# Kernel tuning notes

Hardware: AMD Instinct MI355X
Metric: run time of the kernel (lower is better)

The kernel has to match this reference:

```python
import jax, jax.numpy as jnp
import numpy as np

EMBED_DIM = 128
NUM_HEADS = 8
HEAD_DIM = EMBED_DIM // NUM_HEADS
SCALE = float(np.sqrt(HEAD_DIM))


def setup_inputs() -> dict:
    key = jax.random.key(0)
    ks = jax.random.split(key, 16)
    B, N, M, E = 16, 256, 256, EMBED_DIM
    s = 1.0 / np.sqrt(E)
    inp = {
        "query": jax.random.normal(ks[0], (B, N, E), jnp.float32),
        "key": jax.random.normal(ks[1], (B, M, E), jnp.float32),
        "value": jax.random.normal(ks[2], (B, M, E), jnp.float32),
        "rel_pe": jax.random.normal(ks[3], (B, N, M, E), jnp.float32),
        "attn_mask": jnp.zeros((B, N, M), jnp.float32),
        # linear params stored as [in, out]; y = x @ W + b
        "Wq": jax.random.normal(ks[4], (E, E), jnp.float32) * s,
        "bq": jnp.zeros((E,), jnp.float32),
        "Wk": jax.random.normal(ks[5], (E, E), jnp.float32) * s,
        "bk": jnp.zeros((E,), jnp.float32),
        "Wv": jax.random.normal(ks[6], (E, E), jnp.float32) * s,
        "bv": jnp.zeros((E,), jnp.float32),
        "Wpe": jax.random.normal(ks[7], (E, E), jnp.float32) * s,
        "bpe": jnp.zeros((E,), jnp.float32),
        "Wo": jax.random.normal(ks[8], (E, E), jnp.float32) * s,
        "bo": jnp.zeros((E,), jnp.float32),
    }
    return inp


def reference(query, key, value, rel_pe, attn_mask,
              Wq, bq, Wk, bk, Wv, bv, Wpe, bpe, Wo, bo):
    B, N, E = query.shape
    M = key.shape[1]
    H, D = NUM_HEADS, HEAD_DIM
    q = (query @ Wq + bq).reshape(B, N, H, D)
    k = (key @ Wk + bk).reshape(B, M, H, D)
    v = (value @ Wv + bv).reshape(B, M, H, D)
    pe = (rel_pe @ Wpe + bpe).reshape(B, N, M, H, D)
    score = jnp.einsum('bnhd,bmhd->bhnm', q, k) \
          + jnp.einsum('bnhd,bnmhd->bhnm', q, pe)
    score = score / SCALE + attn_mask[:, None, :, :]
    attn = jax.nn.softmax(score, axis=-1)
    attn = jnp.nan_to_num(attn, nan=0.0)  # dropout is identity in eval mode
    out = jnp.einsum('bhnm,bmhd->bnhd', attn, v) \
        + jnp.einsum('bhnm,bnmhd->bnhd', attn, pe)
    out = out.reshape(B, N, E)
    return out @ Wo + bo
```

## Files before the change

kernel.cpp:

```cpp
#include <hip/hip_runtime.h>
#include <hip/hip_bf16.h>
#include <math.h>

typedef __attribute__((ext_vector_type(8))) short bf16x8;
typedef __attribute__((ext_vector_type(4))) float f32x4;

__device__ __forceinline__ void wg_barrier() {
    asm volatile("s_waitcnt lgkmcnt(0)" ::: "memory");
    __builtin_amdgcn_s_barrier();
    asm volatile("" ::: "memory");
}

__global__ void qkv_proj_kernel(const float* __restrict__ query,
                                const float* __restrict__ key,
                                const float* __restrict__ value,
                                const float* __restrict__ Wq, const float* __restrict__ bq,
                                const float* __restrict__ Wk, const float* __restrict__ bk,
                                const float* __restrict__ Wv, const float* __restrict__ bv,
                                float* __restrict__ qf, float* __restrict__ kf,
                                float* __restrict__ vf)
{
    const int mat = blockIdx.x >> 8;
    const int rb  = blockIdx.x & 255;
    const float* X; const float* W; const float* bias; float* dst;
    if (mat == 0)      { X = query; W = Wq; bias = bq; dst = qf; }
    else if (mat == 1) { X = key;   W = Wk; bias = bk; dst = kf; }
    else               { X = value; W = Wv; bias = bv; dst = vf; }

    __shared__ float sX[16][128];
    const int tid = threadIdx.x;
    const float* src = X + (size_t)rb * 16 * 128;
    #pragma unroll
    for (int i = 0; i < 8; ++i) {
        int idx = tid + i * 256;
        sX[idx >> 7][idx & 127] = src[idx];
    }
    __syncthreads();

    const int col = tid & 127;
    const int rg  = tid >> 7;
    float acc[8] = {0.f,0.f,0.f,0.f,0.f,0.f,0.f,0.f};
    for (int e = 0; e < 128; ++e) {
        float w = W[e * 128 + col];
        #pragma unroll
        for (int r = 0; r < 8; ++r) acc[r] += sX[rg * 8 + r][e] * w;
    }
    float bb = bias[col];
    #pragma unroll
    for (int r = 0; r < 8; ++r)
        dst[(size_t)(rb * 16 + rg * 8 + r) * 128 + col] = acc[r] + bb;
}

__global__ __launch_bounds__(256) void mha_main_kernel(
    const float* __restrict__ relpe,
    const float* __restrict__ mask,
    const float* __restrict__ qf,
    const float* __restrict__ kf,
    const float* __restrict__ vf,
    const float* __restrict__ Wpe, const float* __restrict__ bpe,
    const float* __restrict__ Wo,  const float* __restrict__ bo,
    float* __restrict__ out)
{
    __shared__ __hip_bfloat16 sA[64][140];
    __shared__ __hip_bfloat16 sWt[16][136];
    __shared__ __hip_bfloat16 sPfull[16][264];
    __shared__ float sQK[256][9];
    __shared__ float sQs[128];
    __shared__ float sLw[32];
    __shared__ float sL[8];
    __shared__ float sRed[128];
    __shared__ float sOutF[128];
    __shared__ float sPrE[8][132];

    const int tid  = threadIdx.x;
    const int lane = tid & 63;
    const int wv   = tid >> 6;
    const int bid  = ((blockIdx.x & 7) << 9) | (blockIdx.x >> 3);
    const int b    = bid >> 8;
    const int n    = bid & 255;
    const size_t bn = (size_t)(b * 256 + n);

    float4 pf[8];
    {
        const float4* s4 = (const float4*)(relpe + (bn * 256) * 128);
        #pragma unroll
        for (int i = 0; i < 8; ++i) pf[i] = s4[tid + i * 256];
    }

    if (tid < 128) sQs[tid] = qf[bn * 128 + tid] * 0.25f;
    #pragma unroll
    for (int j = 0; j < 8; ++j) sPfull[8 + j][tid] = __float2bfloat16(0.f);
    if (tid < 128) {
        #pragma unroll
        for (int r = 8; r < 16; ++r) sWt[r][tid] = __float2bfloat16(0.f);
    }
    wg_barrier();

    #pragma unroll
    for (int o = tid; o < 1024; o += 256) {
        int h = o >> 7, e = o & 127;
        const float4* wr = (const float4*)(Wpe + (size_t)e * 128 + h * 16);
        float4 w0 = wr[0], w1 = wr[1], w2 = wr[2], w3 = wr[3];
        const float* qh = &sQs[h * 16];
        float acc = w0.x*qh[0]+w0.y*qh[1]+w0.z*qh[2]+w0.w*qh[3]
                  + w1.x*qh[4]+w1.y*qh[5]+w1.z*qh[6]+w1.w*qh[7]
                  + w2.x*qh[8]+w2.y*qh[9]+w2.z*qh[10]+w2.w*qh[11]
                  + w3.x*qh[12]+w3.y*qh[13]+w3.z*qh[14]+w3.w*qh[15];
        sWt[h][e] = __float2bfloat16(acc);
    }

    {
        const int hsc = tid >> 5, ml = tid & 31;
        float cb = 0.f;
        #pragma unroll
        for (int d = 0; d < 16; ++d) cb += bpe[hsc * 16 + d] * sQs[hsc * 16 + d];
        #pragma unroll
        for (int i = 0; i < 8; ++i) {
            int m = i * 32 + ml;
            const float4* k4 = (const float4*)(kf + ((size_t)(b * 256) + m) * 128 + hsc * 16);
            float4 ka = k4[0], kb = k4[1], kc = k4[2], kd = k4[3];
            const float* qh = &sQs[hsc * 16];
            float s = ka.x*qh[0]+ka.y*qh[1]+ka.z*qh[2]+ka.w*qh[3]
                    + kb.x*qh[4]+kb.y*qh[5]+kb.z*qh[6]+kb.w*qh[7]
                    + kc.x*qh[8]+kc.y*qh[9]+kc.z*qh[10]+kc.w*qh[11]
                    + kd.x*qh[12]+kd.y*qh[13]+kd.z*qh[14]+kd.w*qh[15];
            sQK[m][hsc] = s + cb + mask[bn * 256 + m];
        }
    }

    #pragma unroll
    for (int i = 0; i < 8; ++i) {
        int idx4 = tid + i * 256;
        int lr = idx4 >> 5, c4 = (idx4 & 31) * 4;
        union { __hip_bfloat162 h2[2]; uint2 u; } pk;
        pk.h2[0] = __float22bfloat162_rn(make_float2(pf[i].x, pf[i].y));
        pk.h2[1] = __float22bfloat162_rn(make_float2(pf[i].z, pf[i].w));
        *(uint2*)&sA[lr][c4] = pk.u;
    }
    wg_barrier();

    float l_acc = 0.f;
    f32x4 pr0 = {}, pr1 = {};
    const int arow = lane & 15;
    const int koff = lane >> 4;

    #pragma unroll 1
    for (int t = 0; t < 4; ++t) {
        if (t < 3) {
            const float4* s4 = (const float4*)(relpe + (bn * 256 + (t + 1) * 64) * 128);
            #pragma unroll
            for (int i = 0; i < 8; ++i) pf[i] = s4[tid + i * 256];
        }

        f32x4 cs;
        #pragma unroll
        for (int r = 0; r < 4; ++r) {
            int m = t * 64 + wv * 16 + koff * 4 + r;
            cs[r] = (arow < 8) ? sQK[m][arow] : 0.f;
        }
        #pragma unroll
        for (int kt = 0; kt < 4; ++kt) {
            bf16x8 af  = *(const bf16x8*)&sA[wv * 16 + arow][kt * 32 + koff * 8];
            bf16x8 bfr = *(const bf16x8*)&sWt[arow][kt * 32 + koff * 8];
            cs = __builtin_amdgcn_mfma_f32_16x16x32_bf16(af, bfr, cs, 0, 0, 0);
        }

        if (arow < 8) {
            float p0 = __expf(cs[0]), p1 = __expf(cs[1]);
            float p2 = __expf(cs[2]), p3 = __expf(cs[3]);
            l_acc += (p0 + p1) + (p2 + p3);
            union { __hip_bfloat162 h2[2]; uint2 u; } pk;
            pk.h2[0] = __float22bfloat162_rn(make_float2(p0, p1));
            pk.h2[1] = __float22bfloat162_rn(make_float2(p2, p3));
            *(uint2*)&sPfull[arow][t * 64 + wv * 16 + koff * 4] = pk.u;
        }
        wg_barrier();

        #pragma unroll
        for (int kt = 0; kt < 2; ++kt) {
            bf16x8 ap = *(const bf16x8*)&sPfull[arow][t * 64 + kt * 32 + koff * 8];
            bf16x8 b0, b1;
            #pragma unroll
            for (int j = 0; j < 8; ++j) {
                int row = kt * 32 + koff * 8 + j;
                b0[j] = *(const short*)&sA[row][wv * 32 + arow];
                b1[j] = *(const short*)&sA[row][wv * 32 + 16 + arow];
            }
            pr0 = __builtin_amdgcn_mfma_f32_16x16x32_bf16(ap, b0, pr0, 0, 0, 0);
            pr1 = __builtin_amdgcn_mfma_f32_16x16x32_bf16(ap, b1, pr1, 0, 0, 0);
        }
        wg_barrier();

        if (t < 3) {
            #pragma unroll
            for (int i = 0; i < 8; ++i) {
                int idx4 = tid + i * 256;
                int lr = idx4 >> 5, c4 = (idx4 & 31) * 4;
                union { __hip_bfloat162 h2[2]; uint2 u; } pk;
                pk.h2[0] = __float22bfloat162_rn(make_float2(pf[i].x, pf[i].y));
                pk.h2[1] = __float22bfloat162_rn(make_float2(pf[i].z, pf[i].w));
                *(uint2*)&sA[lr][c4] = pk.u;
            }
            wg_barrier();
        }
    }

    {
        float lw = l_acc;
        lw += __shfl_xor(lw, 16);
        lw += __shfl_xor(lw, 32);
        if (koff == 0 && arow < 8) sLw[wv * 8 + arow] = lw;
    }
    #pragma unroll
    for (int r = 0; r < 4; ++r) {
        int hh = koff * 4 + r;
        if (hh < 8) {
            sPrE[hh][wv * 32 + arow]      = pr0[r];
            sPrE[hh][wv * 32 + 16 + arow] = pr1[r];
        }
    }
    __syncthreads();
    if (tid < 8) sL[tid] = sLw[tid] + sLw[8 + tid] + sLw[16 + tid] + sLw[24 + tid];
    __syncthreads();

    const int e = tid & 127, half = tid >> 7, hh2 = e >> 4;

    float oa = 0.f;
    {
        const float* vp = vf + ((size_t)(b * 256) + half * 128) * 128 + e;
        const __hip_bfloat16* pp = &sPfull[hh2][half * 128];
        #pragma unroll 8
        for (int mm = 0; mm < 128; ++mm)
            oa += __bfloat162float(pp[mm]) * vp[(size_t)mm * 128];
    }
    float ype = 0.f;
    {
        const float* wp  = Wpe + (size_t)(half * 64) * 128 + e;
        const float* prh = &sPrE[hh2][half * 64];
        #pragma unroll 8
        for (int ee = 0; ee < 64; ++ee) ype += prh[ee] * wp[(size_t)ee * 128];
    }
    if (half) sRed[e] = oa + ype;
    __syncthreads();
    if (!half) sOutF[e] = (oa + ype + sRed[e]) / sL[hh2] + bpe[e];
    __syncthreads();

    float y = 0.f;
    {
        const float* wo = Wo + (size_t)(half * 64) * 128 + e;
        #pragma unroll 8
        for (int ee = 0; ee < 64; ++ee) y += sOutF[half * 64 + ee] * wo[(size_t)ee * 128];
    }
    if (half) sRed[e] = y;
    __syncthreads();
    if (!half) out[bn * 128 + e] = y + sRed[e] + bo[e];
}

extern "C" void kernel_launch(void* const* d_in, const int* in_sizes, int n_in,
                              void* d_out, int out_size, void* d_ws, size_t ws_size,
                              hipStream_t stream)
{
    const float* query = (const float*)d_in[0];
    const float* key   = (const float*)d_in[1];
    const float* value = (const float*)d_in[2];
    const float* relpe = (const float*)d_in[3];
    const float* mask  = (const float*)d_in[4];
    const float* Wq  = (const float*)d_in[5];
    const float* bq  = (const float*)d_in[6];
    const float* Wk  = (const float*)d_in[7];
    const float* bk  = (const float*)d_in[8];
    const float* Wv  = (const float*)d_in[9];
    const float* bv  = (const float*)d_in[10];
    const float* Wpe = (const float*)d_in[11];
    const float* bpe = (const float*)d_in[12];
    const float* Wo  = (const float*)d_in[13];
    const float* bo  = (const float*)d_in[14];
    float* out = (float*)d_out;

    float* qf = (float*)d_ws;
    float* kf = qf + 16 * 256 * 128;
    float* vf = kf + 16 * 256 * 128;

    qkv_proj_kernel<<<dim3(768), dim3(256), 0, stream>>>(
        query, key, value, Wq, bq, Wk, bk, Wv, bv, qf, kf, vf);
    mha_main_kernel<<<dim3(4096), dim3(256), 0, stream>>>(
        relpe, mask, qf, kf, vf, Wpe, bpe, Wo, bo, out);
}
```

Before: 224.6 us.

## Stream rel_pe tiles into double-buffered LDS with async global_load_lds

Replaces the register-staged rel_pe prefetch, which converted each tile to bf16 and wrote it into shared memory, with direct global-to-LDS loads of the raw fp32 tiles. The tiles go into two XOR-swizzled buffers, and the bf16 conversion moves to fragment-read time just before each MFMA. A partial vmcnt wait lets the next tile's load overlap the current tile's score and PE-accumulation MFMAs. Score and other scratch arrays are aliased into the buffers, and zero-fill of unused padding rows is dropped. The cost is about 79KB of dynamic shared memory per block, which lowers occupancy, plus repeated fp32-to-bf16 conversion during the strided reads.

```diff
diff --git a/kernel.cpp b/kernel.cpp
--- a/kernel.cpp
+++ b/kernel.cpp
@@ -9,6 +9,22 @@
     asm volatile("s_waitcnt lgkmcnt(0)" ::: "memory");
     __builtin_amdgcn_s_barrier();
     asm volatile("" ::: "memory");
+}
+
+__device__ __forceinline__ bf16x8 pack_f32x8(float4 a, float4 b) {
+    union { __hip_bfloat162 h2[4]; bf16x8 v; } u;
+    u.h2[0] = __float22bfloat162_rn(make_float2(a.x, a.y));
+    u.h2[1] = __float22bfloat162_rn(make_float2(a.z, a.w));
+    u.h2[2] = __float22bfloat162_rn(make_float2(b.x, b.y));
+    u.h2[3] = __float22bfloat162_rn(make_float2(b.z, b.w));
+    return u.v;
+}
+__device__ __forceinline__ bf16x8 pack_f32p(const float* f) {
+    union { __hip_bfloat162 h2[4]; bf16x8 v; } u;
+    #pragma unroll
+    for (int k = 0; k < 4; ++k)
+        u.h2[k] = __float22bfloat162_rn(make_float2(f[2*k], f[2*k+1]));
+    return u.v;
 }
 
 __global__ void qkv_proj_kernel(const float* __restrict__ query,
@@ -40,6 +56,7 @@
     const int col = tid & 127;
     const int rg  = tid >> 7;
     float acc[8] = {0.f,0.f,0.f,0.f,0.f,0.f,0.f,0.f};
+    #pragma unroll 8
     for (int e = 0; e < 128; ++e) {
         float w = W[e * 128 + col];
         #pragma unroll
@@ -50,6 +67,69 @@
     for (int r = 0; r < 8; ++r)
         dst[(size_t)(rb * 16 + rg * 8 + r) * 128 + col] = acc[r] + bb;
 }
+
+
+#define STAGE(dstbuf, gbase)                                                      \
+    {                                                                             \
+        _Pragma("unroll")                                                         \
+        for (int i_ = 0; i_ < 8; ++i_) {                                          \
+            int row_ = (i_ * 4 + wv) * 2 + (lane >> 5);                           \
+            int goff_ = row_ * 512 + (((lane & 31) ^ (row_ & 7)) << 4);           \
+            __builtin_amdgcn_global_load_lds(                                     \
+                (const __attribute__((address_space(1))) void*)((gbase) + goff_), \
+                (__attribute__((address_space(3))) void*)((dstbuf) + (i_ * 4 + wv) * 1024), \
+                16, 0, 0);                                                        \
+        }                                                                         \
+        __builtin_amdgcn_sched_barrier(0);                                        \
+    }
+
+#define TILE_STEP(T, CURB, NXTB, WAITSTR)                                         \
+    {                                                                             \
+        if ((T) < 3) STAGE(NXTB, relpe_b + ((T) + 1) * 32768)                     \
+        asm volatile("s_waitcnt " WAITSTR ::: "memory");                          \
+        __builtin_amdgcn_sched_barrier(0);                                        \
+        wg_barrier();                                                             \
+        const char* bA_ = (CURB);                                                 \
+                                              \
+        f32x4 cs;                                                                 \
+        cs[0] = qkr[(T)*4+0]; cs[1] = qkr[(T)*4+1];                               \
+        cs[2] = qkr[(T)*4+2]; cs[3] = qkr[(T)*4+3];                               \
+        _Pragma("unroll")                                                         \
+        for (int kt = 0; kt < 4; ++kt) {                                          \
+            int u0 = kt * 8 + koff * 2;                                           \
+            float4 fa0 = *(const float4*)(bA_ + rowa_b + ((u0 ^ xr) << 4));       \
+            float4 fa1 = *(const float4*)(bA_ + rowa_b + (((u0 + 1) ^ xr) << 4)); \
+            bf16x8 af = pack_f32x8(fa0, fa1);                                     \
+            bf16x8 bw = *(const bf16x8*)&sWt[arow][kt * 32 + koff * 8];           \
+            cs = __builtin_amdgcn_mfma_f32_16x16x32_bf16(af, bw, cs, 0, 0, 0);    \
+        }                                                                         \
+        if (arow < 8) {                                                           \
+            float p0 = __expf(cs[0]), p1 = __expf(cs[1]);                         \
+            float p2 = __expf(cs[2]), p3 = __expf(cs[3]);                         \
+            l_acc += (p0 + p1) + (p2 + p3);                                       \
+            union { __hip_bfloat162 h2[2]; uint2 u; } pk;                         \
+            pk.h2[0] = __float22bfloat162_rn(make_float2(p0, p1));                \
+            pk.h2[1] = __float22bfloat162_rn(make_float2(p2, p3));                \
+            *(uint2*)&sPfull[arow][(T) * 64 + wv * 16 + koff * 4] = pk.u;         \
+        }                                                                         \
+        wg_barrier();                                                             \
+                                               \
+        _Pragma("unroll")                                                         \
+        for (int kt = 0; kt < 2; ++kt) {                                          \
+            bf16x8 ap = *(const bf16x8*)&sPfull[arow][(T) * 64 + kt * 32 + koff * 8]; \
+            float f0[8], f1[8];                                                   \
+            _Pragma("unroll")                                                     \
+            for (int j = 0; j < 8; ++j) {                                         \
+                int rb_ = kt * 16384 + koff * 4096 + j * 512;                     \
+                f0[j] = *(const float*)(bA_ + rb_ + ((colu0 ^ j) << 4) + colw0);  \
+                f1[j] = *(const float*)(bA_ + rb_ + ((colu1 ^ j) << 4) + colw0);  \
+            }                                                                     \
+            bf16x8 b0 = pack_f32p(f0), b1 = pack_f32p(f1);                        \
+            pr0 = __builtin_amdgcn_mfma_f32_16x16x32_bf16(ap, b0, pr0, 0, 0, 0);  \
+            pr1 = __builtin_amdgcn_mfma_f32_16x16x32_bf16(ap, b1, pr1, 0, 0, 0);  \
+        }                                                                         \
+        wg_barrier();                                                             \
+    }
 
 __global__ __launch_bounds__(256) void mha_main_kernel(
     const float* __restrict__ relpe,
@@ -61,16 +141,14 @@
     const float* __restrict__ Wo,  const float* __restrict__ bo,
     float* __restrict__ out)
 {
-    __shared__ __hip_bfloat16 sA[64][140];
-    __shared__ __hip_bfloat16 sWt[16][136];
-    __shared__ __hip_bfloat16 sPfull[16][264];
-    __shared__ float sQK[256][9];
-    __shared__ float sQs[128];
-    __shared__ float sLw[32];
-    __shared__ float sL[8];
-    __shared__ float sRed[128];
-    __shared__ float sOutF[128];
-    __shared__ float sPrE[8][132];
+    extern __shared__ char smem[];
+    char* buf0 = smem;
+    char* buf1 = smem + 32768;
+    __hip_bfloat16 (*sPfull)[264] = (__hip_bfloat16(*)[264])(smem + 65536);
+    __hip_bfloat16 (*sWt)[136]    = (__hip_bfloat16(*)[136])(smem + 73984);
+    float* sQs = (float*)(smem + 78336);
+    float* sLw = (float*)(smem + 78848);
+    float* sL  = (float*)(smem + 78976);
 
     const int tid  = threadIdx.x;
     const int lane = tid & 63;
@@ -79,21 +157,14 @@
     const int b    = bid >> 8;
     const int n    = bid & 255;
     const size_t bn = (size_t)(b * 256 + n);
-
-    float4 pf[8];
-    {
-        const float4* s4 = (const float4*)(relpe + (bn * 256) * 128);
-        #pragma unroll
-        for (int i = 0; i < 8; ++i) pf[i] = s4[tid + i * 256];
-    }
+    const int arow = lane & 15;
+    const int koff = lane >> 4;
+
+    const char* relpe_b = (const char*)relpe + bn * 131072;
+
+    STAGE(buf0, relpe_b)
 
     if (tid < 128) sQs[tid] = qf[bn * 128 + tid] * 0.25f;
-    #pragma unroll
-    for (int j = 0; j < 8; ++j) sPfull[8 + j][tid] = __float2bfloat16(0.f);
-    if (tid < 128) {
-        #pragma unroll
-        for (int r = 8; r < 16; ++r) sWt[r][tid] = __float2bfloat16(0.f);
-    }
     wg_barrier();
 
     #pragma unroll
@@ -109,6 +180,7 @@
         sWt[h][e] = __float2bfloat16(acc);
     }
 
+    float (*sQK)[9] = (float(*)[9])buf1;
     {
         const int hsc = tid >> 5, ml = tid & 31;
         float cb = 0.f;
@@ -127,83 +199,29 @@
             sQK[m][hsc] = s + cb + mask[bn * 256 + m];
         }
     }
-
-    #pragma unroll
-    for (int i = 0; i < 8; ++i) {
-        int idx4 = tid + i * 256;
-        int lr = idx4 >> 5, c4 = (idx4 & 31) * 4;
-        union { __hip_bfloat162 h2[2]; uint2 u; } pk;
-        pk.h2[0] = __float22bfloat162_rn(make_float2(pf[i].x, pf[i].y));
-        pk.h2[1] = __float22bfloat162_rn(make_float2(pf[i].z, pf[i].w));
-        *(uint2*)&sA[lr][c4] = pk.u;
-    }
+    wg_barrier();
+
+    float qkr[16];
+    #pragma unroll
+    for (int t2 = 0; t2 < 4; ++t2)
+        #pragma unroll
+        for (int r = 0; r < 4; ++r)
+            qkr[t2 * 4 + r] = (arow < 8)
+                ? sQK[t2 * 64 + wv * 16 + koff * 4 + r][arow] : 0.f;
     wg_barrier();
 
     float l_acc = 0.f;
     f32x4 pr0 = {}, pr1 = {};
-    const int arow = lane & 15;
-    const int koff = lane >> 4;
-
-    #pragma unroll 1
-    for (int t = 0; t < 4; ++t) {
-        if (t < 3) {
-            const float4* s4 = (const float4*)(relpe + (bn * 256 + (t + 1) * 64) * 128);
-            #pragma unroll
-            for (int i = 0; i < 8; ++i) pf[i] = s4[tid + i * 256];
-        }
-
-        f32x4 cs;
-        #pragma unroll
-        for (int r = 0; r < 4; ++r) {
-            int m = t * 64 + wv * 16 + koff * 4 + r;
-            cs[r] = (arow < 8) ? sQK[m][arow] : 0.f;
-        }
-        #pragma unroll
-        for (int kt = 0; kt < 4; ++kt) {
-            bf16x8 af  = *(const bf16x8*)&sA[wv * 16 + arow][kt * 32 + koff * 8];
-            bf16x8 bfr = *(const bf16x8*)&sWt[arow][kt * 32 + koff * 8];
-            cs = __builtin_amdgcn_mfma_f32_16x16x32_bf16(af, bfr, cs, 0, 0, 0);
-        }
-
-        if (arow < 8) {
-            float p0 = __expf(cs[0]), p1 = __expf(cs[1]);
-            float p2 = __expf(cs[2]), p3 = __expf(cs[3]);
-            l_acc += (p0 + p1) + (p2 + p3);
-            union { __hip_bfloat162 h2[2]; uint2 u; } pk;
-            pk.h2[0] = __float22bfloat162_rn(make_float2(p0, p1));
-            pk.h2[1] = __float22bfloat162_rn(make_float2(p2, p3));
-            *(uint2*)&sPfull[arow][t * 64 + wv * 16 + koff * 4] = pk.u;
-        }
-        wg_barrier();
-
-        #pragma unroll
-        for (int kt = 0; kt < 2; ++kt) {
-            bf16x8 ap = *(const bf16x8*)&sPfull[arow][t * 64 + kt * 32 + koff * 8];
-            bf16x8 b0, b1;
-            #pragma unroll
-            for (int j = 0; j < 8; ++j) {
-                int row = kt * 32 + koff * 8 + j;
-                b0[j] = *(const short*)&sA[row][wv * 32 + arow];
-                b1[j] = *(const short*)&sA[row][wv * 32 + 16 + arow];
-            }
-            pr0 = __builtin_amdgcn_mfma_f32_16x16x32_bf16(ap, b0, pr0, 0, 0, 0);
-            pr1 = __builtin_amdgcn_mfma_f32_16x16x32_bf16(ap, b1, pr1, 0, 0, 0);
-        }
-        wg_barrier();
-
-        if (t < 3) {
-            #pragma unroll
-            for (int i = 0; i < 8; ++i) {
-                int idx4 = tid + i * 256;
-                int lr = idx4 >> 5, c4 = (idx4 & 31) * 4;
-                union { __hip_bfloat162 h2[2]; uint2 u; } pk;
-                pk.h2[0] = __float22bfloat162_rn(make_float2(pf[i].x, pf[i].y));
-                pk.h2[1] = __float22bfloat162_rn(make_float2(pf[i].z, pf[i].w));
-                *(uint2*)&sA[lr][c4] = pk.u;
-            }
-            wg_barrier();
-        }
-    }
+    const int rowa_b = (wv * 16 + arow) * 512;
+    const int xr     = (wv * 16 + arow) & 7;
+    const int colu0  = (wv * 32 + arow) >> 2;
+    const int colw0  = ((wv * 32 + arow) & 3) * 4;
+    const int colu1  = colu0 + 4;
+
+    TILE_STEP(0, buf0, buf1, "vmcnt(8)")
+    TILE_STEP(1, buf1, buf0, "vmcnt(8)")
+    TILE_STEP(2, buf0, buf1, "vmcnt(8)")
+    TILE_STEP(3, buf1, buf0, "vmcnt(0)")
 
     {
         float lw = l_acc;
@@ -211,12 +229,15 @@
         lw += __shfl_xor(lw, 32);
         if (koff == 0 && arow < 8) sLw[wv * 8 + arow] = lw;
     }
+    float* sPrE = (float*)buf0;
+    float* sRed = (float*)(buf0 + 4352);
+    float* sOutF= (float*)(buf0 + 4864);
     #pragma unroll
     for (int r = 0; r < 4; ++r) {
         int hh = koff * 4 + r;
         if (hh < 8) {
-            sPrE[hh][wv * 32 + arow]      = pr0[r];
-            sPrE[hh][wv * 32 + 16 + arow] = pr1[r];
+            sPrE[hh * 132 + wv * 32 + arow]      = pr0[r];
+            sPrE[hh * 132 + wv * 32 + 16 + arow] = pr1[r];
         }
     }
     __syncthreads();
@@ -236,7 +257,7 @@
     float ype = 0.f;
     {
         const float* wp  = Wpe + (size_t)(half * 64) * 128 + e;
-        const float* prh = &sPrE[hh2][half * 64];
+        const float* prh = &sPrE[hh2 * 132 + half * 64];
         #pragma unroll 8
         for (int ee = 0; ee < 64; ++ee) ype += prh[ee] * wp[(size_t)ee * 128];
     }
@@ -281,8 +302,12 @@
     float* kf = qf + 16 * 256 * 128;
     float* vf = kf + 16 * 256 * 128;
 
+    static bool attr_done = false;
+    (void)hipFuncSetAttribute((const void*)mha_main_kernel,
+                              hipFuncAttributeMaxDynamicSharedMemorySize, 79008);
+
     qkv_proj_kernel<<<dim3(768), dim3(256), 0, stream>>>(
         query, key, value, Wq, bq, Wk, bk, Wv, bv, qf, kf, vf);
-    mha_main_kernel<<<dim3(4096), dim3(256), 0, stream>>>(
+    mha_main_kernel<<<dim3(4096), dim3(256), 79008, stream>>>(
         relpe, mask, qf, kf, vf, Wpe, bpe, Wo, bo, out);
 }
```

After: 259.7 us. 15.6% more time.
